# Optimization experiments

Hardware: AMD Instinct MI355X
Metric: run time of the kernel (lower is better)

The kernel has to match this reference:

```python
import jax, jax.numpy as jnp
import numpy as np

K = 9          # 3x3 deformable kernel positions
EPS = 1e-5     # BatchNorm eps


def conv3x3(x, w, stride=1):
    # x: [B,C,H,W], w: [O,I,3,3], padding=1
    return jax.lax.conv_general_dilated(
        x, w, (stride, stride), ((1, 1), (1, 1)),
        dimension_numbers=('NCHW', 'OIHW', 'NCHW'))


def _bilinear_sample(img, py, px):
    # img: [C,H,W]; py,px: [K,Ho,Wo] float sample coords (zero outside).
    H, W = img.shape[1], img.shape[2]
    y0 = jnp.floor(py)
    x0 = jnp.floor(px)

    def corner(yc, xc):
        w = (1.0 - jnp.abs(py - yc)) * (1.0 - jnp.abs(px - xc))
        valid = (yc >= 0) & (yc <= H - 1) & (xc >= 0) & (xc <= W - 1)
        yi = jnp.clip(yc, 0, H - 1).astype(jnp.int32)
        xi = jnp.clip(xc, 0, W - 1).astype(jnp.int32)
        v = img[:, yi, xi]                      # [C,K,Ho,Wo]
        return v * (w * valid)[None]

    return (corner(y0, x0) + corner(y0, x0 + 1) +
            corner(y0 + 1, x0) + corner(y0 + 1, x0 + 1))


def deform_conv2d(x, offset, mask, w, stride=1, pad=1):
    # x: [B,Cin,H,W]; offset: [B,2K,Ho,Wo] (y,x interleaved per tap);
    # mask: [B,K,Ho,Wo]; w: [Cout,Cin,3,3]. torchvision DCNv2 semantics.
    B, Cin = x.shape[0], x.shape[1]
    Ho, Wo = offset.shape[2], offset.shape[3]
    Cout = w.shape[0]
    kh, kw = jnp.meshgrid(jnp.arange(3), jnp.arange(3), indexing='ij')
    kh = kh.reshape(K).astype(x.dtype)
    kw = kw.reshape(K).astype(x.dtype)
    base_y = (jnp.arange(Ho) * stride - pad).astype(x.dtype)
    base_x = (jnp.arange(Wo) * stride - pad).astype(x.dtype)
    off = offset.reshape(B, K, 2, Ho, Wo)
    py = base_y[None, None, :, None] + kh[None, :, None, None] + off[:, :, 0]
    px = base_x[None, None, None, :] + kw[None, :, None, None] + off[:, :, 1]
    g = jax.vmap(_bilinear_sample)(x, py, px)     # [B,Cin,K,Ho,Wo]
    g = g * mask[:, None]
    return jnp.einsum('bikhw,oik->bohw', g, w.reshape(Cout, Cin, K))


def batchnorm(x, gamma, beta, mean, var):
    # eval-mode BN over channel dim of [B,C,H,W]
    inv = jax.lax.rsqrt(var + EPS) * gamma
    return x * inv[None, :, None, None] + (beta - mean * inv)[None, :, None, None]


def setup_inputs() -> dict:
    key = jax.random.key(0)
    ks = jax.random.split(key, 20)
    B, Cin, H, W = 16, 64, 64, 64
    C1, C2, NC = 128, 128, 1000
    inp = {
        'x': jax.random.normal(ks[0], (B, Cin, H, W), jnp.float32),
        'conv1_w': jax.random.normal(ks[1], (C1, Cin, 3, 3), jnp.float32) * 0.05,
        'off1_w': jax.random.normal(ks[2], (2 * K, Cin, 3, 3), jnp.float32) * 0.02,
        'mod1_w': jax.random.normal(ks[3], (K, Cin, 3, 3), jnp.float32) * 0.05,
        'bn1_g': jax.random.uniform(ks[4], (C1,), jnp.float32, 0.5, 1.5),
        'bn1_b': jax.random.normal(ks[5], (C1,), jnp.float32) * 0.1,
        'bn1_m': jax.random.normal(ks[6], (C1,), jnp.float32) * 0.1,
        'bn1_v': jax.random.uniform(ks[7], (C1,), jnp.float32, 0.5, 1.5),
        'conv2_w': jax.random.normal(ks[8], (C2, C1, 3, 3), jnp.float32) * 0.05,
        'off2_w': jax.random.normal(ks[9], (2 * K, C1, 3, 3), jnp.float32) * 0.02,
        'mod2_w': jax.random.normal(ks[10], (K, C1, 3, 3), jnp.float32) * 0.05,
        'bn2_g': jax.random.uniform(ks[11], (C2,), jnp.float32, 0.5, 1.5),
        'bn2_b': jax.random.normal(ks[12], (C2,), jnp.float32) * 0.1,
        'bn2_m': jax.random.normal(ks[13], (C2,), jnp.float32) * 0.1,
        'bn2_v': jax.random.uniform(ks[14], (C2,), jnp.float32, 0.5, 1.5),
        'fc_w': jax.random.normal(ks[15], (NC, C2), jnp.float32) * 0.05,
        'fc_b': jnp.zeros((NC,), jnp.float32),
    }
    return inp


def reference(x, conv1_w, off1_w, mod1_w, bn1_g, bn1_b, bn1_m, bn1_v,
              conv2_w, off2_w, mod2_w, bn2_g, bn2_b, bn2_m, bn2_v,
              fc_w, fc_b):
    stride = 1
    # stage 1: deformable conv (offset + sigmoid modulation) + BN + ReLU
    off = conv3x3(x, off1_w, stride)
    mask = jax.nn.sigmoid(conv3x3(x, mod1_w, stride))
    out = deform_conv2d(x, off, mask, conv1_w, stride=stride, pad=1)
    out = jax.nn.relu(batchnorm(out, bn1_g, bn1_b, bn1_m, bn1_v))
    # stage 2: deformable conv + BN (no ReLU before GAP, as in source)
    off = conv3x3(out, off2_w, stride)
    mask = jax.nn.sigmoid(conv3x3(out, mod2_w, stride))
    out = deform_conv2d(out, off, mask, conv2_w, stride=stride, pad=1)
    out = batchnorm(out, bn2_g, bn2_b, bn2_m, bn2_v)
    # global average pool + fc
    out = out.mean(axis=(2, 3))                 # [B, C2]
    return out @ fc_w.T + fc_b
```

## Files before the change

kernel.cpp:

```cpp
#include <hip/hip_runtime.h>

#define TPB 256
typedef unsigned short us;
typedef __attribute__((ext_vector_type(8))) _Float16 f16x8;
typedef __attribute__((ext_vector_type(2))) _Float16 f16x2;
typedef __attribute__((ext_vector_type(4))) float f32x4;

__device__ inline us f2h(float f){ union{ _Float16 h; us u; } x; x.h = (_Float16)f; return x.u; }
__device__ inline f16x2 u2h2(unsigned u){ union{ unsigned v; f16x2 h; } x; x.v = u; return x.h; }
#define MFMA16(a,b,c) __builtin_amdgcn_mfma_f32_16x16x32_f16((a),(b),(c),0,0,0)

__global__ __launch_bounds__(256) void k_transpose_x(const float* __restrict__ x,
                                                     us* __restrict__ xT){
  __shared__ float tile[64][65];
  const int y = blockIdx.x, b = blockIdx.y;
  for (int i = threadIdx.x; i < 4096; i += TPB){
    const int c = i >> 6, xx = i & 63;
    tile[c][xx] = x[b*262144 + c*4096 + y*64 + xx];
  }
  __syncthreads();
  for (int i = threadIdx.x; i < 4096; i += TPB){
    const int xx = i >> 6, c = i & 63;
    xT[(size_t)(b*4096 + y*64 + xx)*64 + c] = f2h(tile[c][xx]);
  }
}

__global__ __launch_bounds__(256) void k_prep(
    const float* __restrict__ cw1, const float* __restrict__ ow1, const float* __restrict__ mw1,
    const float* __restrict__ cw2, const float* __restrict__ ow2, const float* __restrict__ mw2,
    us* __restrict__ d1, us* __restrict__ d2, us* __restrict__ a1, us* __restrict__ a2){
  const int e = blockIdx.x*TPB + threadIdx.x;
  if (e < 73728){
    int k = e/8192, r = e%8192, kb = r/4096, r2 = r%4096;
    int n0 = r2>>9, q = r2&511, l = q>>3, j = q&7;
    int co = n0*16 + (l&15), c = kb*32 + (l>>4)*8 + j;
    d1[e] = f2h(cw1[(co*64 + c)*9 + k]);
  }
  if (e < 147456){
    int k = e/16384, r = e%16384, kb = r/4096, r2 = r%4096;
    int n0 = r2>>9, q = r2&511, l = q>>3, j = q&7;
    int co = n0*16 + (l&15), c = kb*32 + (l>>4)*8 + j;
    d2[e] = f2h(cw2[(co*128 + c)*9 + k]);
  }
  if (e < 18432){
    int k = e/2048, r = e%2048, kb = r/1024, r2 = r%1024;
    int n0 = r2>>9, q = r2&511, l = q>>3, j = q&7;
    int co = n0*16 + (l&15), c = kb*32 + (l>>4)*8 + j;
    float w = (co < 18) ? ow1[(co*64 + c)*9 + k] : (co < 27 ? mw1[((co-18)*64 + c)*9 + k] : 0.f);
    a1[e] = f2h(w);
  }
  if (e < 36864){
    int k = e/4096, r = e%4096, kb = r/1024, r2 = r%1024;
    int n0 = r2>>9, q = r2&511, l = q>>3, j = q&7;
    int co = n0*16 + (l&15), c = kb*32 + (l>>4)*8 + j;
    float w = (co < 18) ? ow2[(co*128 + c)*9 + k] : (co < 27 ? mw2[((co-18)*128 + c)*9 + k] : 0.f);
    a2[e] = f2h(w);
  }
}

template<int CIN, int STAGE>
__global__ __launch_bounds__(512, 4) void k_fused(
    const us* __restrict__ inT,
    const us* __restrict__ wb_aux, const us* __restrict__ wb_def,
    const float* __restrict__ bn_g, const float* __restrict__ bn_b,
    const float* __restrict__ bn_m, const float* __restrict__ bn_v,
    us* __restrict__ outT, float* __restrict__ partial){
  constexpr int KB2  = CIN/64;
  constexpr int NC   = 9*KB2;
  constexpr int WE_A = 2*(CIN/32)*512;
  constexpr int WE_D = 8*(CIN/32)*512;

  __shared__ __align__(16) us pool[12672];
  __shared__ uint4 otab[576];
  __shared__ uint2 wtab[576];
  __shared__ float extra[256];

  const int id  = blockIdx.x;
  const int nid = (id & 7)*128 + (id >> 3);
  const int b = nid >> 6, ho = nid & 63;
  const int tid = threadIdx.x;
  const us* __restrict__ inb = inT + (size_t)b*4096*CIN;
  const char* __restrict__ inbc = (const char*)inb;

  if (STAGE == 1 && tid < 128){
    float inv = rsqrtf(bn_v[tid] + 1e-5f)*bn_g[tid];
    extra[tid] = inv; extra[128 + tid] = bn_b[tid] - bn_m[tid]*inv;
  }

  const int lane = tid & 63, lr = lane & 15, lg = lane >> 4;
  const int wv = tid >> 6;
  const int mh = wv & 3, nh = wv >> 2;

  f32x4 aacc = (f32x4){0.f,0.f,0.f,0.f};
  auto load_rows = [&](int kb2, uint4* rq){
    #pragma unroll
    for (int it = 0; it < 4; ++it){
      const int s = it*512 + tid;
      if (s < 1584){
        const int slot = s >> 3, cq = s & 7;
        const int r = slot/66, p = slot - r*66;
        const int y = ho - 1 + r, x = p - 1;
        rq[it] = make_uint4(0u,0u,0u,0u);
        if (y >= 0 && y < 64 && x >= 0 && x < 64)
          rq[it] = *(const uint4*)(inb + (size_t)(y*64 + x)*CIN + kb2*64 + cq*8);
      }
    }
  };
  auto write_rows = [&](const uint4* rq){
    #pragma unroll
    for (int it = 0; it < 4; ++it){
      const int s = it*512 + tid;
      if (s < 1584){
        const int slot = s >> 3, cq = s & 7;
        *(uint4*)(pool + slot*64 + ((cq ^ (slot & 7))*8)) = rq[it];
      }
    }
  };
  auto mfma_aux = [&](int kb2){
    #pragma unroll
    for (int k = 0; k < 9; ++k){
      const int kh = k/3, kw = k - kh*3;
      const int slot = kh*66 + mh*16 + lr + kw;
      #pragma unroll
      for (int kbl = 0; kbl < 2; ++kbl){
        f16x8 a = *(const f16x8*)(pool + slot*64 + (((kbl*4 + lg) ^ (slot & 7))*8));
        f16x8 bf = *(const f16x8*)(wb_aux + (size_t)k*WE_A + (size_t)((kb2*2 + kbl)*2 + nh)*512 + lane*8);
        aacc = MFMA16(a, bf, aacc);
      }
    }
  };
  {
    uint4 rqA[4], rqB[4];
    load_rows(0, rqA);
    write_rows(rqA);
    if constexpr (KB2 == 2) load_rows(1, rqB);
    __syncthreads();
    mfma_aux(0);
    if constexpr (KB2 == 2){
      __syncthreads();
      write_rows(rqB);
      __syncthreads();
      mfma_aux(1);
    }
  }
  __syncthreads();

  float* am = (float*)pool;
  {
    const int co = nh*16 + lr;
    if (co < 27){
      #pragma unroll
      for (int i = 0; i < 4; ++i) am[co*66 + mh*16 + lg*4 + i] = aacc[i];
    }
  }
  __syncthreads();

  for (int sid = tid; sid < 576; sid += 512){
    const int k = sid >> 6, px = sid & 63;
    const int kh = k/3, kw = k - kh*3;
    float oy = am[(2*k)*66 + px];
    float ox = am[(2*k+1)*66 + px];
    float mv = 1.f/(1.f + expf(-am[(18+k)*66 + px]));
    float py  = (float)(ho - 1 + kh) + oy;
    float pxx = (float)(px - 1 + kw) + ox;
    float fyf = floorf(py), fxf = floorf(pxx);
    int y0 = (int)fyf, x0 = (int)fxf;
    float dy = py - fyf, dx = pxx - fxf;
    bool vy0 = (y0 >= 0) && (y0 < 64), vy1 = (y0 >= -1) && (y0 < 63);
    bool vx0 = (x0 >= 0) && (x0 < 64), vx1 = (x0 >= -1) && (x0 < 63);
    int y0c = min(max(y0,0),63), y1c = min(max(y0+1,0),63);
    int x0c = min(max(x0,0),63), x1c = min(max(x0+1,0),63);
    const unsigned str = CIN*2u;
    otab[sid] = make_uint4((unsigned)(y0c*64 + x0c)*str, (unsigned)(y0c*64 + x1c)*str,
                           (unsigned)(y1c*64 + x0c)*str, (unsigned)(y1c*64 + x1c)*str);
    float w00 = (1.f-dy)*(1.f-dx)*mv*((vy0 && vx0) ? 1.f : 0.f);
    float w01 = (1.f-dy)*dx     *mv*((vy0 && vx1) ? 1.f : 0.f);
    float w10 = dy*(1.f-dx)     *mv*((vy1 && vx0) ? 1.f : 0.f);
    float w11 = dy*dx           *mv*((vy1 && vx1) ? 1.f : 0.f);
    wtab[sid] = make_uint2((unsigned)f2h(w00) | ((unsigned)f2h(w01) << 16),
                           (unsigned)f2h(w10) | ((unsigned)f2h(w11) << 16));
  }
  __syncthreads();

  f32x4 acc[4];
  #pragma unroll
  for (int m = 0; m < 4; ++m) acc[m] = (f32x4){0.f,0.f,0.f,0.f};

  const int pxs = tid >> 3, cqs = tid & 7;

  auto load_corners = [&](int i, f16x8* cr){
    const int k = i/KB2, kb2 = i - (i/KB2)*KB2;
    const uint4 o = otab[k*64 + pxs];
    const unsigned c0 = (unsigned)(kb2*64 + cqs*8)*2u;
    cr[0] = *(const f16x8*)(inbc + o.x + c0);
    cr[1] = *(const f16x8*)(inbc + o.y + c0);
    cr[2] = *(const f16x8*)(inbc + o.z + c0);
    cr[3] = *(const f16x8*)(inbc + o.w + c0);
  };
  auto load_B = [&](int i, f16x8* bbp){
    const int k = i/KB2, kb2 = i - (i/KB2)*KB2;
    #pragma unroll
    for (int kbl = 0; kbl < 2; ++kbl)
      bbp[kbl] = *(const f16x8*)(wb_def + (size_t)k*WE_D + (size_t)((kb2*2 + kbl)*8 + wv)*512 + lane*8);
  };
  auto blend_write = [&](int i, const f16x8* cr, us* dst){
    const int k = i/KB2;
    const uint2 wp = wtab[k*64 + pxs];
    const f16x2 wAB = u2h2(wp.x), wCD = u2h2(wp.y);
    const _Float16 wA = wAB[0], wB = wAB[1], wC = wCD[0], wD = wCD[1];
    const f16x8 va = (f16x8){wA,wA,wA,wA,wA,wA,wA,wA};
    const f16x8 vb = (f16x8){wB,wB,wB,wB,wB,wB,wB,wB};
    const f16x8 vc = (f16x8){wC,wC,wC,wC,wC,wC,wC,wC};
    const f16x8 vd = (f16x8){wD,wD,wD,wD,wD,wD,wD,wD};
    f16x8 r = cr[0]*va + cr[1]*vb;
    r = r + cr[2]*vc + cr[3]*vd;
    *(f16x8*)(dst + pxs*64 + ((cqs ^ (pxs & 7))*8)) = r;
  };
  auto mfma_def = [&](int i, const us* src, const f16x8* bbp){
    #pragma unroll
    for (int kbl = 0; kbl < 2; ++kbl){
      #pragma unroll
      for (int mt = 0; mt < 4; ++mt){
        const int row = mt*16 + lr;
        f16x8 a = *(const f16x8*)(src + row*64 + (((kbl*4 + lg) ^ (row & 7))*8));
        acc[mt] = MFMA16(a, bbp[kbl], acc[mt]);
      }
    }
  };

  us* g0 = pool;
  us* g1 = pool + 4096;
  f16x8 crA[4], crB[4], bbA[2], bbB[2];
  load_corners(0, crA); load_B(0, bbA);
  load_corners(1, crB); load_B(1, bbB);
  blend_write(0, crA, g0);
  __syncthreads();
  for (int ii = 0; ii < NC; ii += 2){
    if (ii + 2 < NC) load_corners(ii+2, crA);
    mfma_def(ii, g0, bbA);
    if (ii + 2 < NC) load_B(ii+2, bbA);
    if (ii + 1 < NC) blend_write(ii+1, crB, g1);
    __syncthreads();
    if (ii + 1 < NC){
      if (ii + 3 < NC) load_corners(ii+3, crB);
      mfma_def(ii+1, g1, bbB);
      if (ii + 3 < NC) load_B(ii+3, bbB);
      if (ii + 2 < NC) blend_write(ii+2, crA, g0);
      __syncthreads();
    }
  }

  if (STAGE == 1){
    const size_t rowbase = (size_t)(b*4096 + ho*64)*128;
    const int co = wv*16 + lr;
    const float inv = extra[co], bia = extra[128 + co];
    #pragma unroll
    for (int mt = 0; mt < 4; ++mt){
      const int pxl = mt*16 + lg*4;
      #pragma unroll
      for (int i = 0; i < 4; ++i){
        float v = acc[mt][i]*inv + bia;
        outT[rowbase + (size_t)(pxl + i)*128 + co] = f2h(fmaxf(v, 0.f));
      }
    }
  } else {
    float s = 0.f;
    #pragma unroll
    for (int mt = 0; mt < 4; ++mt)
      s += acc[mt][0] + acc[mt][1] + acc[mt][2] + acc[mt][3];
    s += __shfl_xor(s, 16);
    s += __shfl_xor(s, 32);
    if (lane < 16) extra[wv*16 + lane] = s;
    __syncthreads();
    if (tid < 128) partial[(size_t)(b*64 + ho)*128 + tid] = extra[tid];
  }
}

__global__ __launch_bounds__(256) void k_pool(
    const float* __restrict__ partial,
    const float* __restrict__ g2, const float* __restrict__ b2,
    const float* __restrict__ m2, const float* __restrict__ v2,
    float* __restrict__ pooled){
  const int t = blockIdx.x*TPB + threadIdx.x;
  if (t >= 2048) return;
  const int b = t >> 7, c = t & 127;
  float s = 0.f;
  for (int h = 0; h < 64; ++h) s += partial[(b*64 + h)*128 + c];
  const float inv = rsqrtf(v2[c] + 1e-5f)*g2[c];
  pooled[t] = s*(1.f/4096.f)*inv + (b2[c] - m2[c]*inv);
}

__global__ __launch_bounds__(256) void k_fc(
    const float* __restrict__ pooled, const float* __restrict__ fcw,
    const float* __restrict__ fcb, float* __restrict__ outp){
  const int t = blockIdx.x*TPB + threadIdx.x;
  if (t >= 16000) return;
  const int b = t/1000, n = t - b*1000;
  const float* p = pooled + b*128;
  const float* w = fcw + n*128;
  float s = fcb[n];
  #pragma unroll
  for (int c = 0; c < 128; c += 4){
    const float4 pv = *(const float4*)(p + c);
    const float4 wv = *(const float4*)(w + c);
    s = fmaf(pv.x, wv.x, s); s = fmaf(pv.y, wv.y, s);
    s = fmaf(pv.z, wv.z, s); s = fmaf(pv.w, wv.w, s);
  }
  outp[t] = s;
}

extern "C" void kernel_launch(void* const* d_in, const int* in_sizes, int n_in,
                              void* d_out, int out_size, void* d_ws, size_t ws_size,
                              hipStream_t stream){
  const float* x      = (const float*)d_in[0];
  const float* conv1w = (const float*)d_in[1];
  const float* off1w  = (const float*)d_in[2];
  const float* mod1w  = (const float*)d_in[3];
  const float* bn1g   = (const float*)d_in[4];
  const float* bn1b   = (const float*)d_in[5];
  const float* bn1m   = (const float*)d_in[6];
  const float* bn1v   = (const float*)d_in[7];
  const float* conv2w = (const float*)d_in[8];
  const float* off2w  = (const float*)d_in[9];
  const float* mod2w  = (const float*)d_in[10];
  const float* bn2g   = (const float*)d_in[11];
  const float* bn2b   = (const float*)d_in[12];
  const float* bn2m   = (const float*)d_in[13];
  const float* bn2v   = (const float*)d_in[14];
  const float* fcw    = (const float*)d_in[15];
  const float* fcb    = (const float*)d_in[16];

  char* w = (char*)d_ws;
  us*    xT      = (us*)(w);
  us*    out1T   = (us*)(w + 8388608);
  float* partial = (float*)(w + 25165824);
  float* pooled  = (float*)(w + 25690112);
  us*    wb_d1   = (us*)(w + 25698304);
  us*    wb_d2   = (us*)(w + 25845760);
  us*    wb_a1   = (us*)(w + 26140672);
  us*    wb_a2   = (us*)(w + 26177536);

  k_transpose_x<<<dim3(64,16), TPB, 0, stream>>>(x, xT);
  k_prep<<<576, TPB, 0, stream>>>(conv1w, off1w, mod1w, conv2w, off2w, mod2w,
                                  wb_d1, wb_d2, wb_a1, wb_a2);

  k_fused<64,1><<<1024, 512, 0, stream>>>(
      xT, wb_a1, wb_d1, bn1g, bn1b, bn1m, bn1v, out1T, nullptr);
  k_fused<128,2><<<1024, 512, 0, stream>>>(
      out1T, wb_a2, wb_d2, nullptr, nullptr, nullptr, nullptr, nullptr, partial);

  k_pool<<<8, TPB, 0, stream>>>(partial, bn2g, bn2b, bn2m, bn2v, pooled);
  k_fc<<<63, TPB, 0, stream>>>(pooled, fcw, fcb, (float*)d_out);
}
```

Measured before the change: 96.37 us.

## Split fused deform-conv blocks into half-row tiles and stage stage-1 output through LDS

```diff
diff --git a/kernel.cpp b/kernel.cpp
--- a/kernel.cpp
+++ b/kernel.cpp
@@ -59,7 +59,7 @@
 }
 
 template<int CIN, int STAGE>
-__global__ __launch_bounds__(512, 4) void k_fused(
+__global__ __launch_bounds__(256, 6) void k_fused(
     const us* __restrict__ inT,
     const us* __restrict__ wb_aux, const us* __restrict__ wb_def,
     const float* __restrict__ bn_g, const float* __restrict__ bn_b,
@@ -70,14 +70,15 @@
   constexpr int WE_A = 2*(CIN/32)*512;
   constexpr int WE_D = 8*(CIN/32)*512;
 
-  __shared__ __align__(16) us pool[12672];
-  __shared__ uint4 otab[576];
-  __shared__ uint2 wtab[576];
+  __shared__ __align__(16) us pool[6528];
+  __shared__ uint4 otab[288];
+  __shared__ uint2 wtab[288];
   __shared__ float extra[256];
 
-  const int id  = blockIdx.x;
-  const int nid = (id & 7)*128 + (id >> 3);
-  const int b = nid >> 6, ho = nid & 63;
+  const int bid = blockIdx.x;
+  const int nid = (bid & 7)*256 + (bid >> 3);
+  const int b = nid >> 7, ho = (nid >> 1) & 63, hh = nid & 1;
+  const int px0 = hh*32;
   const int tid = threadIdx.x;
   const us* __restrict__ inb = inT + (size_t)b*4096*CIN;
   const char* __restrict__ inbc = (const char*)inb;
@@ -89,17 +90,17 @@
 
   const int lane = tid & 63, lr = lane & 15, lg = lane >> 4;
   const int wv = tid >> 6;
-  const int mh = wv & 3, nh = wv >> 2;
+  const int mh = wv & 1, nh = wv >> 1;
 
   f32x4 aacc = (f32x4){0.f,0.f,0.f,0.f};
   auto load_rows = [&](int kb2, uint4* rq){
     #pragma unroll
     for (int it = 0; it < 4; ++it){
-      const int s = it*512 + tid;
-      if (s < 1584){
+      const int s = it*256 + tid;
+      if (s < 816){
         const int slot = s >> 3, cq = s & 7;
-        const int r = slot/66, p = slot - r*66;
-        const int y = ho - 1 + r, x = p - 1;
+        const int r = slot/34, p = slot - r*34;
+        const int y = ho - 1 + r, x = px0 + p - 1;
         rq[it] = make_uint4(0u,0u,0u,0u);
         if (y >= 0 && y < 64 && x >= 0 && x < 64)
           rq[it] = *(const uint4*)(inb + (size_t)(y*64 + x)*CIN + kb2*64 + cq*8);
@@ -109,8 +110,8 @@
   auto write_rows = [&](const uint4* rq){
     #pragma unroll
     for (int it = 0; it < 4; ++it){
-      const int s = it*512 + tid;
-      if (s < 1584){
+      const int s = it*256 + tid;
+      if (s < 816){
         const int slot = s >> 3, cq = s & 7;
         *(uint4*)(pool + slot*64 + ((cq ^ (slot & 7))*8)) = rq[it];
       }
@@ -120,7 +121,7 @@
     #pragma unroll
     for (int k = 0; k < 9; ++k){
       const int kh = k/3, kw = k - kh*3;
-      const int slot = kh*66 + mh*16 + lr + kw;
+      const int slot = kh*34 + mh*16 + lr + kw;
       #pragma unroll
       for (int kbl = 0; kbl < 2; ++kbl){
         f16x8 a = *(const f16x8*)(pool + slot*64 + (((kbl*4 + lg) ^ (slot & 7))*8));
@@ -150,19 +151,19 @@
     const int co = nh*16 + lr;
     if (co < 27){
       #pragma unroll
-      for (int i = 0; i < 4; ++i) am[co*66 + mh*16 + lg*4 + i] = aacc[i];
-    }
-  }
-  __syncthreads();
-
-  for (int sid = tid; sid < 576; sid += 512){
-    const int k = sid >> 6, px = sid & 63;
+      for (int i = 0; i < 4; ++i) am[co*33 + mh*16 + lg*4 + i] = aacc[i];
+    }
+  }
+  __syncthreads();
+
+  for (int sid = tid; sid < 288; sid += 256){
+    const int k = sid >> 5, px = sid & 31;
     const int kh = k/3, kw = k - kh*3;
-    float oy = am[(2*k)*66 + px];
-    float ox = am[(2*k+1)*66 + px];
-    float mv = 1.f/(1.f + expf(-am[(18+k)*66 + px]));
+    float oy = am[(2*k)*33 + px];
+    float ox = am[(2*k+1)*33 + px];
+    float mv = 1.f/(1.f + expf(-am[(18+k)*33 + px]));
     float py  = (float)(ho - 1 + kh) + oy;
-    float pxx = (float)(px - 1 + kw) + ox;
+    float pxx = (float)(px0 + px - 1 + kw) + ox;
     float fyf = floorf(py), fxf = floorf(pxx);
     int y0 = (int)fyf, x0 = (int)fxf;
     float dy = py - fyf, dx = pxx - fxf;
@@ -182,15 +183,15 @@
   }
   __syncthreads();
 
-  f32x4 acc[4];
+  f32x4 acc[2][2];
   #pragma unroll
-  for (int m = 0; m < 4; ++m) acc[m] = (f32x4){0.f,0.f,0.f,0.f};
+  for (int m = 0; m < 2; ++m){ acc[m][0] = (f32x4){0.f,0.f,0.f,0.f}; acc[m][1] = (f32x4){0.f,0.f,0.f,0.f}; }
 
   const int pxs = tid >> 3, cqs = tid & 7;
 
   auto load_corners = [&](int i, f16x8* cr){
     const int k = i/KB2, kb2 = i - (i/KB2)*KB2;
-    const uint4 o = otab[k*64 + pxs];
+    const uint4 o = otab[k*32 + pxs];
     const unsigned c0 = (unsigned)(kb2*64 + cqs*8)*2u;
     cr[0] = *(const f16x8*)(inbc + o.x + c0);
     cr[1] = *(const f16x8*)(inbc + o.y + c0);
@@ -201,11 +202,14 @@
     const int k = i/KB2, kb2 = i - (i/KB2)*KB2;
     #pragma unroll
     for (int kbl = 0; kbl < 2; ++kbl)
-      bbp[kbl] = *(const f16x8*)(wb_def + (size_t)k*WE_D + (size_t)((kb2*2 + kbl)*8 + wv)*512 + lane*8);
+      #pragma unroll
+      for (int nt = 0; nt < 2; ++nt)
+        bbp[kbl*2 + nt] = *(const f16x8*)(wb_def + (size_t)k*WE_D
+                          + (size_t)((kb2*2 + kbl)*8 + wv*2 + nt)*512 + lane*8);
   };
   auto blend_write = [&](int i, const f16x8* cr, us* dst){
     const int k = i/KB2;
-    const uint2 wp = wtab[k*64 + pxs];
+    const uint2 wp = wtab[k*32 + pxs];
     const f16x2 wAB = u2h2(wp.x), wCD = u2h2(wp.y);
     const _Float16 wA = wAB[0], wB = wAB[1], wC = wCD[0], wD = wCD[1];
     const f16x8 va = (f16x8){wA,wA,wA,wA,wA,wA,wA,wA};
@@ -220,17 +224,18 @@
     #pragma unroll
     for (int kbl = 0; kbl < 2; ++kbl){
       #pragma unroll
-      for (int mt = 0; mt < 4; ++mt){
+      for (int mt = 0; mt < 2; ++mt){
         const int row = mt*16 + lr;
         f16x8 a = *(const f16x8*)(src + row*64 + (((kbl*4 + lg) ^ (row & 7))*8));
-        acc[mt] = MFMA16(a, bbp[kbl], acc[mt]);
+        acc[mt][0] = MFMA16(a, bbp[kbl*2 + 0], acc[mt][0]);
+        acc[mt][1] = MFMA16(a, bbp[kbl*2 + 1], acc[mt][1]);
       }
     }
   };
 
   us* g0 = pool;
-  us* g1 = pool + 4096;
-  f16x8 crA[4], crB[4], bbA[2], bbB[2];
+  us* g1 = pool + 2048;
+  f16x8 crA[4], crB[4], bbA[4], bbB[4];
   load_corners(0, crA); load_B(0, bbA);
   load_corners(1, crB); load_B(1, bbB);
   blend_write(0, crA, g0);
@@ -251,28 +256,43 @@
   }
 
   if (STAGE == 1){
-    const size_t rowbase = (size_t)(b*4096 + ho*64)*128;
-    const int co = wv*16 + lr;
-    const float inv = extra[co], bia = extra[128 + co];
-    #pragma unroll
-    for (int mt = 0; mt < 4; ++mt){
-      const int pxl = mt*16 + lg*4;
-      #pragma unroll
-      for (int i = 0; i < 4; ++i){
-        float v = acc[mt][i]*inv + bia;
-        outT[rowbase + (size_t)(pxl + i)*128 + co] = f2h(fmaxf(v, 0.f));
-      }
+    #pragma unroll
+    for (int mt = 0; mt < 2; ++mt){
+      #pragma unroll
+      for (int nt = 0; nt < 2; ++nt){
+        const int co = (wv*2 + nt)*16 + lr;
+        const float inv = extra[co], bia = extra[128 + co];
+        const int grp = co >> 3, rem = co & 7;
+        #pragma unroll
+        for (int i = 0; i < 4; ++i){
+          const int px = mt*16 + lg*4 + i;
+          float v = acc[mt][nt][i]*inv + bia;
+          pool[px*128 + (((grp ^ (px & 7)) << 3) | rem)] = f2h(fmaxf(v, 0.f));
+        }
+      }
+    }
+    __syncthreads();
+    const size_t base = ((size_t)(b*4096 + ho*64 + px0))*128;
+    #pragma unroll
+    for (int it = 0; it < 2; ++it){
+      const int idx = it*256 + tid;
+      const int p = idx >> 4, g = idx & 15;
+      *(uint4*)(outT + base + p*128 + g*8) =
+          *(const uint4*)(pool + p*128 + (((g ^ (p & 7)) << 3)));
     }
   } else {
-    float s = 0.f;
-    #pragma unroll
-    for (int mt = 0; mt < 4; ++mt)
-      s += acc[mt][0] + acc[mt][1] + acc[mt][2] + acc[mt][3];
-    s += __shfl_xor(s, 16);
-    s += __shfl_xor(s, 32);
-    if (lane < 16) extra[wv*16 + lane] = s;
+    #pragma unroll
+    for (int nt = 0; nt < 2; ++nt){
+      float s = 0.f;
+      #pragma unroll
+      for (int mt = 0; mt < 2; ++mt)
+        s += acc[mt][nt][0] + acc[mt][nt][1] + acc[mt][nt][2] + acc[mt][nt][3];
+      s += __shfl_xor(s, 16);
+      s += __shfl_xor(s, 32);
+      if (lane < 16) extra[(wv*2 + nt)*16 + lane] = s;
+    }
     __syncthreads();
-    if (tid < 128) partial[(size_t)(b*64 + ho)*128 + tid] = extra[tid];
+    if (tid < 128) partial[(size_t)nid*128 + tid] = extra[tid];
   }
 }
 
@@ -285,7 +305,7 @@
   if (t >= 2048) return;
   const int b = t >> 7, c = t & 127;
   float s = 0.f;
-  for (int h = 0; h < 64; ++h) s += partial[(b*64 + h)*128 + c];
+  for (int h = 0; h < 128; ++h) s += partial[(size_t)(b*128 + h)*128 + c];
   const float inv = rsqrtf(v2[c] + 1e-5f)*g2[c];
   pooled[t] = s*(1.f/4096.f)*inv + (b2[c] - m2[c]*inv);
 }
@@ -334,19 +354,19 @@
   us*    xT      = (us*)(w);
   us*    out1T   = (us*)(w + 8388608);
   float* partial = (float*)(w + 25165824);
-  float* pooled  = (float*)(w + 25690112);
-  us*    wb_d1   = (us*)(w + 25698304);
-  us*    wb_d2   = (us*)(w + 25845760);
-  us*    wb_a1   = (us*)(w + 26140672);
-  us*    wb_a2   = (us*)(w + 26177536);
+  float* pooled  = (float*)(w + 26214400);
+  us*    wb_d1   = (us*)(w + 26222592);
+  us*    wb_d2   = (us*)(w + 26370048);
+  us*    wb_a1   = (us*)(w + 26664960);
+  us*    wb_a2   = (us*)(w + 26701824);
 
   k_transpose_x<<<dim3(64,16), TPB, 0, stream>>>(x, xT);
   k_prep<<<576, TPB, 0, stream>>>(conv1w, off1w, mod1w, conv2w, off2w, mod2w,
                                   wb_d1, wb_d2, wb_a1, wb_a2);
 
-  k_fused<64,1><<<1024, 512, 0, stream>>>(
+  k_fused<64,1><<<2048, TPB, 0, stream>>>(
       xT, wb_a1, wb_d1, bn1g, bn1b, bn1m, bn1v, out1T, nullptr);
-  k_fused<128,2><<<1024, 512, 0, stream>>>(
+  k_fused<128,2><<<2048, TPB, 0, stream>>>(
       out1T, wb_a2, wb_d2, nullptr, nullptr, nullptr, nullptr, nullptr, partial);
 
   k_pool<<<8, TPB, 0, stream>>>(partial, bn2g, bn2b, bn2m, bn2v, pooled);
```

Measured after the change: 172.2 us. 1.79x slower.

## Blend samples directly into MFMA A-fragments and split K across waves

Applied to the files above, without the earlier changes.

```diff
diff --git a/kernel.cpp b/kernel.cpp
--- a/kernel.cpp
+++ b/kernel.cpp
@@ -182,97 +182,109 @@
   }
   __syncthreads();
 
-  f32x4 acc[4];
+  const int mt = wv & 3, kblh = wv >> 2;
+  const int pxw = mt*16 + lr;
+  const unsigned cofs = (unsigned)((kblh*32 + lg*8)*2);
+
+  f32x4 acc[8];
   #pragma unroll
-  for (int m = 0; m < 4; ++m) acc[m] = (f32x4){0.f,0.f,0.f,0.f};
-
-  const int pxs = tid >> 3, cqs = tid & 7;
+  for (int n = 0; n < 8; ++n) acc[n] = (f32x4){0.f,0.f,0.f,0.f};
 
   auto load_corners = [&](int i, f16x8* cr){
     const int k = i/KB2, kb2 = i - (i/KB2)*KB2;
-    const uint4 o = otab[k*64 + pxs];
-    const unsigned c0 = (unsigned)(kb2*64 + cqs*8)*2u;
+    const uint4 o = otab[k*64 + pxw];
+    const unsigned c0 = (unsigned)(kb2*128) + cofs;
     cr[0] = *(const f16x8*)(inbc + o.x + c0);
     cr[1] = *(const f16x8*)(inbc + o.y + c0);
     cr[2] = *(const f16x8*)(inbc + o.z + c0);
     cr[3] = *(const f16x8*)(inbc + o.w + c0);
   };
-  auto load_B = [&](int i, f16x8* bbp){
+  auto do_chunk = [&](int i, const f16x8* cr){
     const int k = i/KB2, kb2 = i - (i/KB2)*KB2;
-    #pragma unroll
-    for (int kbl = 0; kbl < 2; ++kbl)
-      bbp[kbl] = *(const f16x8*)(wb_def + (size_t)k*WE_D + (size_t)((kb2*2 + kbl)*8 + wv)*512 + lane*8);
-  };
-  auto blend_write = [&](int i, const f16x8* cr, us* dst){
-    const int k = i/KB2;
-    const uint2 wp = wtab[k*64 + pxs];
+    const int kb = kb2*2 + kblh;
+    const uint2 wp = wtab[k*64 + pxw];
     const f16x2 wAB = u2h2(wp.x), wCD = u2h2(wp.y);
     const _Float16 wA = wAB[0], wB = wAB[1], wC = wCD[0], wD = wCD[1];
     const f16x8 va = (f16x8){wA,wA,wA,wA,wA,wA,wA,wA};
     const f16x8 vb = (f16x8){wB,wB,wB,wB,wB,wB,wB,wB};
     const f16x8 vc = (f16x8){wC,wC,wC,wC,wC,wC,wC,wC};
     const f16x8 vd = (f16x8){wD,wD,wD,wD,wD,wD,wD,wD};
-    f16x8 r = cr[0]*va + cr[1]*vb;
-    r = r + cr[2]*vc + cr[3]*vd;
-    *(f16x8*)(dst + pxs*64 + ((cqs ^ (pxs & 7))*8)) = r;
-  };
-  auto mfma_def = [&](int i, const us* src, const f16x8* bbp){
-    #pragma unroll
-    for (int kbl = 0; kbl < 2; ++kbl){
+    f16x8 a = cr[0]*va + cr[1]*vb;
+    a = a + cr[2]*vc + cr[3]*vd;
+    const us* bbase = wb_def + (size_t)k*WE_D + (size_t)(kb*8)*512 + lane*8;
+    #pragma unroll
+    for (int g = 0; g < 2; ++g){
+      f16x8 bf0 = *(const f16x8*)(bbase + (g*4 + 0)*512);
+      f16x8 bf1 = *(const f16x8*)(bbase + (g*4 + 1)*512);
+      f16x8 bf2 = *(const f16x8*)(bbase + (g*4 + 2)*512);
+      f16x8 bf3 = *(const f16x8*)(bbase + (g*4 + 3)*512);
+      acc[g*4 + 0] = MFMA16(a, bf0, acc[g*4 + 0]);
+      acc[g*4 + 1] = MFMA16(a, bf1, acc[g*4 + 1]);
+      acc[g*4 + 2] = MFMA16(a, bf2, acc[g*4 + 2]);
+      acc[g*4 + 3] = MFMA16(a, bf3, acc[g*4 + 3]);
+    }
+  };
+
+  {
+    f16x8 crA[4], crB[4];
+    load_corners(0, crA);
+    for (int ii = 0; ii < NC; ii += 2){
+      if (ii + 1 < NC) load_corners(ii+1, crB);
+      do_chunk(ii, crA);
+      if (ii + 2 < NC) load_corners(ii+2, crA);
+      if (ii + 1 < NC) do_chunk(ii+1, crB);
+    }
+  }
+
+  if (STAGE == 1){
+    float* red = (float*)pool;
+    #pragma unroll
+    for (int r = 0; r < 2; ++r){
+      __syncthreads();
+      if (kblh == 1 && (mt >> 1) == r){
+        #pragma unroll
+        for (int nt = 0; nt < 8; ++nt)
+          *(f32x4*)&red[(((mt & 1)*8 + nt)*64 + lane)*4] = acc[nt];
+      }
+      __syncthreads();
+      if (kblh == 0 && (mt >> 1) == r){
+        #pragma unroll
+        for (int nt = 0; nt < 8; ++nt){
+          f32x4 p = *(const f32x4*)&red[(((mt & 1)*8 + nt)*64 + lane)*4];
+          acc[nt] += p;
+        }
+      }
+    }
+    if (kblh == 0){
+      const size_t rowbase = (size_t)(b*4096 + ho*64)*128;
       #pragma unroll
-      for (int mt = 0; mt < 4; ++mt){
-        const int row = mt*16 + lr;
-        f16x8 a = *(const f16x8*)(src + row*64 + (((kbl*4 + lg) ^ (row & 7))*8));
-        acc[mt] = MFMA16(a, bbp[kbl], acc[mt]);
-      }
-    }
-  };
-
-  us* g0 = pool;
-  us* g1 = pool + 4096;
-  f16x8 crA[4], crB[4], bbA[2], bbB[2];
-  load_corners(0, crA); load_B(0, bbA);
-  load_corners(1, crB); load_B(1, bbB);
-  blend_write(0, crA, g0);
-  __syncthreads();
-  for (int ii = 0; ii < NC; ii += 2){
-    if (ii + 2 < NC) load_corners(ii+2, crA);
-    mfma_def(ii, g0, bbA);
-    if (ii + 2 < NC) load_B(ii+2, bbA);
-    if (ii + 1 < NC) blend_write(ii+1, crB, g1);
+      for (int nt = 0; nt < 8; ++nt){
+        const int co = nt*16 + lr;
+        const float inv = extra[co], bia = extra[128 + co];
+        #pragma unroll
+        for (int i = 0; i < 4; ++i){
+          const int px = mt*16 + lg*4 + i;
+          outT[rowbase + (size_t)px*128 + co] = f2h(fmaxf(acc[nt][i]*inv + bia, 0.f));
+        }
+      }
+    }
+  } else {
+    float* red = (float*)pool;
     __syncthreads();
-    if (ii + 1 < NC){
-      if (ii + 3 < NC) load_corners(ii+3, crB);
-      mfma_def(ii+1, g1, bbB);
-      if (ii + 3 < NC) load_B(ii+3, bbB);
-      if (ii + 2 < NC) blend_write(ii+2, crA, g0);
-      __syncthreads();
-    }
-  }
-
-  if (STAGE == 1){
-    const size_t rowbase = (size_t)(b*4096 + ho*64)*128;
-    const int co = wv*16 + lr;
-    const float inv = extra[co], bia = extra[128 + co];
-    #pragma unroll
-    for (int mt = 0; mt < 4; ++mt){
-      const int pxl = mt*16 + lg*4;
+    #pragma unroll
+    for (int nt = 0; nt < 8; ++nt){
+      float s = acc[nt][0] + acc[nt][1] + acc[nt][2] + acc[nt][3];
+      s += __shfl_xor(s, 16);
+      s += __shfl_xor(s, 32);
+      if (lane < 16) red[wv*128 + nt*16 + lane] = s;
+    }
+    __syncthreads();
+    if (tid < 128){
+      float s = 0.f;
       #pragma unroll
-      for (int i = 0; i < 4; ++i){
-        float v = acc[mt][i]*inv + bia;
-        outT[rowbase + (size_t)(pxl + i)*128 + co] = f2h(fmaxf(v, 0.f));
-      }
-    }
-  } else {
-    float s = 0.f;
-    #pragma unroll
-    for (int mt = 0; mt < 4; ++mt)
-      s += acc[mt][0] + acc[mt][1] + acc[mt][2] + acc[mt][3];
-    s += __shfl_xor(s, 16);
-    s += __shfl_xor(s, 32);
-    if (lane < 16) extra[wv*16 + lane] = s;
-    __syncthreads();
-    if (tid < 128) partial[(size_t)(b*64 + ho)*128 + tid] = extra[tid];
+      for (int w8 = 0; w8 < 8; ++w8) s += red[w8*128 + tid];
+      partial[(size_t)(b*64 + ho)*128 + tid] = s;
+    }
   }
 }
 
```

Result: slower. 185.9 us (+92.9%).
